# Performance work log

Hardware: AMD Instinct MI355X
Metric: run time of the kernel (lower is better)

Reference implementation:

```python
import jax, jax.numpy as jnp
import numpy as np

DEPTH = 6
H = 12
D = 768
FF = 4 * D
OUT_INDICES = (2, 5)
EPS = 1e-5


def layernorm(x, g, b):
    m = jnp.mean(x, axis=-1, keepdims=True)
    v = jnp.mean(jnp.square(x - m), axis=-1, keepdims=True)
    return (x - m) * jax.lax.rsqrt(v + EPS) * g + b


def setup_inputs() -> dict:
    key = jax.random.key(0)
    ks = jax.random.split(key, 8)
    B, N = 2, 1024
    s = 0.02
    inp = {
        "x": jax.random.normal(ks[0], (B, N, D), dtype=jnp.float32),
        "rel_bias": jax.random.normal(ks[1], (H, N, N), dtype=jnp.float32),
        "ln1_g": jnp.ones((DEPTH, D), jnp.float32),
        "ln1_b": jnp.zeros((DEPTH, D), jnp.float32),
        "qkv_w": jax.random.normal(ks[2], (DEPTH, D, 3 * D), dtype=jnp.float32) * s,
        "out_w": jax.random.normal(ks[3], (DEPTH, D, D), dtype=jnp.float32) * s,
        "out_b": jnp.zeros((DEPTH, D), jnp.float32),
        "ln2_g": jnp.ones((DEPTH, D), jnp.float32),
        "ln2_b": jnp.zeros((DEPTH, D), jnp.float32),
        "ff1_w": jax.random.normal(ks[4], (DEPTH, D, FF), dtype=jnp.float32) * s,
        "ff1_b": jnp.zeros((DEPTH, FF), jnp.float32),
        "ff2_w": jax.random.normal(ks[5], (DEPTH, FF, D), dtype=jnp.float32) * s,
        "ff2_b": jnp.zeros((DEPTH, D), jnp.float32),
        "lnf_g": jnp.ones((D,), jnp.float32),
        "lnf_b": jnp.zeros((D,), jnp.float32),
    }
    return inp


def reference(x, rel_bias, ln1_g, ln1_b, qkv_w, out_w, out_b, ln2_g, ln2_b,
              ff1_w, ff1_b, ff2_w, ff2_b, lnf_g, lnf_b):
    B, N, Dm = x.shape
    Dh = Dm // H
    scale = Dh ** -0.5
    kside = int(round(N ** 0.5))  # N is a perfect square (patch grid)
    feats = []
    for i in range(DEPTH):
        # --- attention block ---
        h = layernorm(x, ln1_g[i], ln1_b[i])
        qkv = h @ qkv_w[i]                                   # [B,N,3D]
        q, k, v = jnp.split(qkv, 3, axis=-1)
        q = q.reshape(B, N, H, Dh).transpose(0, 2, 1, 3)     # [B,H,N,Dh]
        k = k.reshape(B, N, H, Dh).transpose(0, 2, 1, 3)
        v = v.reshape(B, N, H, Dh).transpose(0, 2, 1, 3)
        scores = jnp.einsum('bhid,bhjd->bhij', q, k) * scale + rel_bias
        attn = jax.nn.softmax(scores, axis=-1)
        o = jnp.einsum('bhij,bhjd->bhid', attn, v)
        o = o.transpose(0, 2, 1, 3).reshape(B, N, Dm)
        x = x + (o @ out_w[i] + out_b[i])
        # --- FFN block ---
        h2 = layernorm(x, ln2_g[i], ln2_b[i])
        ff = jax.nn.gelu(h2 @ ff1_w[i] + ff1_b[i], approximate=False)
        x = x + (ff @ ff2_w[i] + ff2_b[i])
        if i in OUT_INDICES:
            feats.append(x.reshape(B, kside, kside, Dm).transpose(0, 3, 1, 2))
    xf = layernorm(x, lnf_g, lnf_b)
    return (xf, *feats)
```

## Files before the change

### kernel.cpp

```cpp
#include <hip/hip_runtime.h>
#include <hip/hip_bf16.h>

typedef unsigned short ushort_t;
typedef __attribute__((ext_vector_type(8))) __bf16 bf16x8;
typedef __attribute__((ext_vector_type(8))) unsigned short u16x8;
typedef __attribute__((ext_vector_type(4))) float f32x4;
typedef __attribute__((ext_vector_type(4))) unsigned int u32x4;

#define DEPTH 6
#define HEADS 12
#define DMODEL 768
#define FFDIM 3072
#define BATCH 2
#define SEQ 1024
#define ROWS (BATCH * SEQ)

static __device__ __forceinline__ ushort_t f2bf(float f) {
  unsigned u = __builtin_bit_cast(unsigned, f);
  u += 0x7fffu + ((u >> 16) & 1u);
  return (ushort_t)(u >> 16);
}
static __device__ __forceinline__ float bf2f(ushort_t v) {
  return __builtin_bit_cast(float, (unsigned)v << 16);
}

template <int MREP, int NREP, int EPI>
__global__ __launch_bounds__(256) void gemm_bt(
    const ushort_t* __restrict__ A, const ushort_t* __restrict__ Bt,
    int lda, int ldb, int K,
    void* __restrict__ out0, void* __restrict__ out1,
    const float* __restrict__ f0) {
  constexpr int BM = 32 * MREP;
  constexpr int BN = 32 * NREP;
  constexpr int CHA = BM / 32;
  constexpr int CHB = BN / 32;
  __shared__ ushort_t sA[2][BM * 64];
  __shared__ ushort_t sB[2][BN * 64];

  const int tid = threadIdx.x;
  const int lane = tid & 63;
  const int wid = tid >> 6;
  const int wm = wid >> 1, wn = wid & 1;

  int bx, by;
  {
    const int nb = gridDim.x * gridDim.y;
    const int bid = blockIdx.y * gridDim.x + blockIdx.x;
    const int q = nb >> 3;
    const int swz = (bid & 7) * q + (bid >> 3);
    bx = swz % gridDim.x;
    by = swz / gridDim.x;
  }

  const ushort_t* Ab = A + (long)bx * BM * lda;
  const ushort_t* Bb = Bt + (long)by * BN * ldb;

  const int srow = lane >> 3;
  const int scol = ((lane & 7) ^ srow) * 8;

  f32x4 acc[MREP][NREP];
#pragma unroll
  for (int m = 0; m < MREP; ++m)
#pragma unroll
    for (int n = 0; n < NREP; ++n) acc[m][n] = (f32x4){0.f, 0.f, 0.f, 0.f};

  const int fr = lane & 15;
  const int kq4 = lane >> 4;

  auto stage_tile = [&](int buf, int t) {
    const int k0 = t * 64;
#pragma unroll
    for (int j = 0; j < CHA; ++j) {
      const int c = wid * CHA + j;
      const ushort_t* src = Ab + (long)(c * 8 + srow) * lda + k0 + scol;
      __builtin_amdgcn_global_load_lds(
          (const __attribute__((address_space(1))) void*)src,
          (__attribute__((address_space(3))) void*)&sA[buf][c * 512], 16, 0, 0);
    }
#pragma unroll
    for (int j = 0; j < CHB; ++j) {
      const int c = wid * CHB + j;
      const ushort_t* src = Bb + (long)(c * 8 + srow) * ldb + k0 + scol;
      __builtin_amdgcn_global_load_lds(
          (const __attribute__((address_space(1))) void*)src,
          (__attribute__((address_space(3))) void*)&sB[buf][c * 512], 16, 0, 0);
    }
  };

  const int nt = K / 64;
  stage_tile(0, 0);
  for (int t = 0; t < nt; ++t) {
    const int cur = t & 1;
    asm volatile("s_waitcnt vmcnt(0)" ::: "memory");
    __builtin_amdgcn_s_barrier();
    if (t + 1 < nt) stage_tile(cur ^ 1, t + 1);
#pragma unroll
    for (int kk = 0; kk < 2; ++kk) {
      bf16x8 af[MREP], bfr[NREP];
#pragma unroll
      for (int m = 0; m < MREP; ++m) {
        const int row = wm * (MREP * 16) + m * 16 + fr;
        const int ch = (kk * 4 + kq4) ^ (row & 7);
        af[m] = *(const bf16x8*)&sA[cur][row * 64 + ch * 8];
      }
#pragma unroll
      for (int n = 0; n < NREP; ++n) {
        const int row = wn * (NREP * 16) + n * 16 + fr;
        const int ch = (kk * 4 + kq4) ^ (row & 7);
        bfr[n] = *(const bf16x8*)&sB[cur][row * 64 + ch * 8];
      }
#pragma unroll
      for (int m = 0; m < MREP; ++m)
#pragma unroll
        for (int n = 0; n < NREP; ++n)
          acc[m][n] = __builtin_amdgcn_mfma_f32_16x16x32_bf16(
              af[m], bfr[n], acc[m][n], 0, 0, 0);
    }
  }

  const long grow0 = (long)bx * BM + wm * (MREP * 16);
  const long gcol0 = (long)by * BN + wn * (NREP * 16);
  const int rr = (lane >> 4) * 4;
  const int cc = lane & 15;

#pragma unroll
  for (int m = 0; m < MREP; ++m) {
#pragma unroll
    for (int n = 0; n < NREP; ++n) {
#pragma unroll
      for (int r = 0; r < 4; ++r) {
        long row = grow0 + m * 16 + rr + r;
        long col = gcol0 + n * 16 + cc;
        float c = acc[m][n][r];
        if (EPI == 0) {
          ushort_t bv = f2bf(c);
          if (col < 1536) {
            ((ushort_t*)out0)[row * 2304 + col] = bv;
          } else {
            long h = (col - 1536) >> 6, d = (col - 1536) & 63;
            long b = row >> 10, i = row & 1023;
            ((ushort_t*)out1)[(((b * HEADS) + h) * 64 + d) * 1024 + i] = bv;
          }
        } else if (EPI == 3) {
          long idx = row * DMODEL + col;
          ((float*)out0)[idx] += c + f0[col];
        } else if (EPI == 4) {
          float t = c + f0[col];
          float g = 0.5f * t * (1.0f + erff(t * 0.70710678118f));
          ((ushort_t*)out0)[row * FFDIM + col] = f2bf(g);
        } else if (EPI == 5) {
          long idx = row * DMODEL + col;
          ((float*)out0)[idx] += c + f0[col];
        }
      }
    }
  }
}

__global__ __launch_bounds__(256) void pack_bias(const float* __restrict__ rel,
                                                 ushort_t* __restrict__ pb) {
  __shared__ ushort_t tile[1024];
  const int blk = blockIdx.x;
  const int t = blk & 15, qi = (blk >> 4) & 63, h = blk >> 10;
  const float* src = rel + ((size_t)h << 20) + (size_t)(qi * 16) * 1024 + t * 64;
  const int tid = threadIdx.x;
  const int kk = tid & 63;
#pragma unroll
  for (int it = 0; it < 4; ++it) {
    const int qr = (tid >> 6) * 4 + it;
    const float v = src[(size_t)qr * 1024 + kk];
    const int lane = (qr >> 2) * 16 + (kk & 15);
    const int idx = (kk >> 4) * 4 + (qr & 3);
    tile[lane * 16 + idx] = f2bf(v);
  }
  __syncthreads();
  ushort_t* dst = pb + (size_t)blk * 1024;
#pragma unroll
  for (int it = 0; it < 4; ++it) dst[it * 256 + tid] = tile[it * 256 + tid];
}

__global__ __launch_bounds__(128) void flash_attn(
    const ushort_t* __restrict__ qkv,
    const ushort_t* __restrict__ vt,
    const ushort_t* __restrict__ pbias,
    ushort_t* __restrict__ o) {
  __shared__ ushort_t sK[2][64 * 64];
  __shared__ ushort_t sV[2][64 * 64];
  __shared__ ushort_t sP[32 * 64];

  const int tid = threadIdx.x;
  const int lane = tid & 63;
  const int wid = tid >> 6;
  const int h = blockIdx.y, b = blockIdx.z;
  const int q0 = blockIdx.x * 32;
  const int qi = blockIdx.x * 2 + wid;

  const int fr = lane & 15;
  const int kq4 = lane >> 4;
  const int rr = kq4 * 4;
  const int cc = fr;

  const int srow = lane >> 3;
  const int scol = ((lane & 7) ^ srow) * 8;

  const ushort_t* qbase =
      qkv + (size_t)(b * 1024 + q0 + wid * 16 + fr) * 2304 + h * 64;
  bf16x8 qreg[2];
  qreg[0] = *(const bf16x8*)&qbase[kq4 * 8];
  qreg[1] = *(const bf16x8*)&qbase[32 + kq4 * 8];

  const ushort_t* Kbase = qkv + (size_t)(b * 1024) * 2304 + 768 + h * 64;
  const ushort_t* Vbase = vt + (size_t)((b * HEADS + h) * 64) * 1024;
  const ushort_t* pbb = pbias + (((size_t)h * 64 + qi) << 14) + lane * 16;

  f32x4 acc_o[4];
  float m_run[4], l_run[4];
#pragma unroll
  for (int n = 0; n < 4; ++n) acc_o[n] = (f32x4){0.f, 0.f, 0.f, 0.f};
#pragma unroll
  for (int r = 0; r < 4; ++r) { m_run[r] = -1e30f; l_run[r] = 0.f; }

  auto stage_kv = [&](int buf, int t) {
#pragma unroll
    for (int j = 0; j < 4; ++j) {
      const int c = wid * 4 + j;
      const ushort_t* src = Kbase + (size_t)(t * 64 + c * 8 + srow) * 2304 + scol;
      __builtin_amdgcn_global_load_lds(
          (const __attribute__((address_space(1))) void*)src,
          (__attribute__((address_space(3))) void*)&sK[buf][c * 512], 16, 0, 0);
    }
#pragma unroll
    for (int j = 0; j < 4; ++j) {
      const int c = wid * 4 + j;
      const ushort_t* src = Vbase + (size_t)(c * 8 + srow) * 1024 + t * 64 + scol;
      __builtin_amdgcn_global_load_lds(
          (const __attribute__((address_space(1))) void*)src,
          (__attribute__((address_space(3))) void*)&sV[buf][c * 512], 16, 0, 0);
    }
  };

  auto step = [&](int t, u16x8& bc0, u16x8& bc1, u16x8& bn0, u16x8& bn1) {
    const int cur = t & 1;
    asm volatile("s_waitcnt vmcnt(0)" ::: "memory");
    __builtin_amdgcn_s_barrier();
    if (t + 1 < 16) {
      stage_kv(cur ^ 1, t + 1);
      const ushort_t* pp = pbb + (size_t)(t + 1) * 1024;
      bn0 = *(const u16x8*)pp;
      bn1 = *(const u16x8*)(pp + 8);
    }

    f32x4 s[4];
#pragma unroll
    for (int n = 0; n < 4; ++n) s[n] = (f32x4){0.f, 0.f, 0.f, 0.f};
#pragma unroll
    for (int kk = 0; kk < 2; ++kk) {
#pragma unroll
      for (int n = 0; n < 4; ++n) {
        const int row = n * 16 + fr;
        const int ch = (kk * 4 + kq4) ^ (row & 7);
        bf16x8 kf = *(const bf16x8*)&sK[cur][row * 64 + ch * 8];
        s[n] =
            __builtin_amdgcn_mfma_f32_16x16x32_bf16(qreg[kk], kf, s[n], 0, 0, 0);
      }
    }

    float mr[4];
#pragma unroll
    for (int r = 0; r < 4; ++r) mr[r] = -1e30f;
#pragma unroll
    for (int n = 0; n < 4; ++n)
#pragma unroll
      for (int r = 0; r < 4; ++r) {
        const int idx = n * 4 + r;
        const float bv = bf2f(idx < 8 ? bc0[idx] : bc1[idx - 8]);
        float v = s[n][r] * 0.125f + bv;
        s[n][r] = v;
        mr[r] = fmaxf(mr[r], v);
      }
#pragma unroll
    for (int o_ = 1; o_ < 16; o_ <<= 1)
#pragma unroll
      for (int r = 0; r < 4; ++r) mr[r] = fmaxf(mr[r], __shfl_xor(mr[r], o_));

    float escale[4], psum[4];
#pragma unroll
    for (int r = 0; r < 4; ++r) {
      float mn = fmaxf(m_run[r], mr[r]);
      escale[r] = __expf(m_run[r] - mn);
      m_run[r] = mn;
      psum[r] = 0.f;
    }
#pragma unroll
    for (int n = 0; n < 4; ++n)
#pragma unroll
      for (int r = 0; r < 4; ++r) {
        float p = __expf(s[n][r] - m_run[r]);
        psum[r] += p;
        const int prow = wid * 16 + rr + r;
        const int pcol = n * 16 + cc;
        sP[prow * 64 + (((pcol >> 3) ^ (prow & 7)) << 3) + (pcol & 7)] = f2bf(p);
      }
#pragma unroll
    for (int o_ = 1; o_ < 16; o_ <<= 1)
#pragma unroll
      for (int r = 0; r < 4; ++r) psum[r] += __shfl_xor(psum[r], o_);
#pragma unroll
    for (int r = 0; r < 4; ++r) l_run[r] = l_run[r] * escale[r] + psum[r];

    asm volatile("s_waitcnt lgkmcnt(0)" ::: "memory");
    __builtin_amdgcn_s_barrier();

#pragma unroll
    for (int n = 0; n < 4; ++n)
#pragma unroll
      for (int r = 0; r < 4; ++r) acc_o[n][r] *= escale[r];
#pragma unroll
    for (int kk = 0; kk < 2; ++kk) {
      const int prow = wid * 16 + fr;
      const int pch = (kk * 4 + kq4) ^ (prow & 7);
      bf16x8 pf = *(const bf16x8*)&sP[prow * 64 + pch * 8];
#pragma unroll
      for (int n = 0; n < 4; ++n) {
        const int vrow = n * 16 + fr;
        const int vch = (kk * 4 + kq4) ^ (vrow & 7);
        bf16x8 vf = *(const bf16x8*)&sV[cur][vrow * 64 + vch * 8];
        acc_o[n] =
            __builtin_amdgcn_mfma_f32_16x16x32_bf16(pf, vf, acc_o[n], 0, 0, 0);
      }
    }
  };

  u16x8 bA0, bA1, bB0, bB1;
  bA0 = *(const u16x8*)pbb;
  bA1 = *(const u16x8*)(pbb + 8);
  stage_kv(0, 0);
  for (int tt = 0; tt < 16; tt += 2) {
    step(tt, bA0, bA1, bB0, bB1);
    step(tt + 1, bB0, bB1, bA0, bA1);
  }

  ushort_t* ob = o + (size_t)(b * 1024 + q0 + wid * 16) * 768 + h * 64;
#pragma unroll
  for (int r = 0; r < 4; ++r) {
    const float rinv = 1.f / l_run[r];
#pragma unroll
    for (int n = 0; n < 4; ++n)
      ob[(size_t)(rr + r) * 768 + n * 16 + cc] = f2bf(acc_o[n][r] * rinv);
  }
}

__global__ __launch_bounds__(256) void transpose_cast(
    const float* __restrict__ in, ushort_t* __restrict__ out, int R, int C) {
  __shared__ float t[32][33];
  const float* ip = in + (long)blockIdx.z * R * C;
  ushort_t* op = out + (long)blockIdx.z * R * C;
  int c0 = blockIdx.x * 32, r0 = blockIdx.y * 32;
  int tx = threadIdx.x;
  for (int i = threadIdx.y; i < 32; i += 8)
    t[i][tx] = ip[(long)(r0 + i) * C + c0 + tx];
  __syncthreads();
  for (int i = threadIdx.y; i < 32; i += 8)
    op[(long)(c0 + i) * R + r0 + tx] = f2bf(t[tx][i]);
}

__global__ __launch_bounds__(256) void ln_kernel(
    const float* __restrict__ x, const float* __restrict__ g,
    const float* __restrict__ b, void* __restrict__ out, int out_f32) {
  int row = blockIdx.x;
  int tid = threadIdx.x;
  int lane = tid & 63, wid = tid >> 6;
  const float* xr = x + (long)row * DMODEL;
  float v0 = xr[tid], v1 = xr[tid + 256], v2 = xr[tid + 512];
  float s = v0 + v1 + v2;
  __shared__ float red[8];
  for (int o = 32; o; o >>= 1) s += __shfl_xor(s, o);
  if (!lane) red[wid] = s;
  __syncthreads();
  float mean = (red[0] + red[1] + red[2] + red[3]) * (1.f / 768.f);
  float d0 = v0 - mean, d1 = v1 - mean, d2 = v2 - mean;
  float q = d0 * d0 + d1 * d1 + d2 * d2;
  for (int o = 32; o; o >>= 1) q += __shfl_xor(q, o);
  if (!lane) red[4 + wid] = q;
  __syncthreads();
  float var = (red[4] + red[5] + red[6] + red[7]) * (1.f / 768.f);
  float rs = rsqrtf(var + 1e-5f);
  float y0 = d0 * rs * g[tid] + b[tid];
  float y1 = d1 * rs * g[tid + 256] + b[tid + 256];
  float y2 = d2 * rs * g[tid + 512] + b[tid + 512];
  if (out_f32) {
    float* o_ = (float*)out + (long)row * DMODEL;
    o_[tid] = y0; o_[tid + 256] = y1; o_[tid + 512] = y2;
  } else {
    ushort_t* o_ = (ushort_t*)out + (long)row * DMODEL;
    o_[tid] = f2bf(y0); o_[tid + 256] = f2bf(y1); o_[tid + 512] = f2bf(y2);
  }
}

__global__ __launch_bounds__(256) void feat_kernel(const float* __restrict__ x,
                                                   float* __restrict__ out) {
  __shared__ float t[32][33];
  const float* xp = x + (long)blockIdx.z * SEQ * DMODEL;
  float* op = out + (long)blockIdx.z * DMODEL * SEQ;
  int n0 = blockIdx.x * 32, c0 = blockIdx.y * 32;
  int tx = threadIdx.x;
  for (int i = threadIdx.y; i < 32; i += 8)
    t[i][tx] = xp[(long)(n0 + i) * DMODEL + c0 + tx];
  __syncthreads();
  for (int i = threadIdx.y; i < 32; i += 8)
    op[(long)(c0 + i) * SEQ + n0 + tx] = t[tx][i];
}

extern "C" void kernel_launch(void* const* d_in, const int* in_sizes, int n_in,
                              void* d_out, int out_size, void* d_ws,
                              size_t ws_size, hipStream_t stream) {
  const float* x_in   = (const float*)d_in[0];
  const float* rel    = (const float*)d_in[1];
  const float* ln1_g  = (const float*)d_in[2];
  const float* ln1_b  = (const float*)d_in[3];
  const float* qkv_w  = (const float*)d_in[4];
  const float* out_w  = (const float*)d_in[5];
  const float* out_b  = (const float*)d_in[6];
  const float* ln2_g  = (const float*)d_in[7];
  const float* ln2_b  = (const float*)d_in[8];
  const float* ff1_w  = (const float*)d_in[9];
  const float* ff1_b  = (const float*)d_in[10];
  const float* ff2_w  = (const float*)d_in[11];
  const float* ff2_b  = (const float*)d_in[12];
  const float* lnf_g  = (const float*)d_in[13];
  const float* lnf_b  = (const float*)d_in[14];
  float* out = (float*)d_out;

  char* w = (char*)d_ws;
  ushort_t* wq_t = (ushort_t*)w; w += (size_t)DEPTH * 2304 * 768 * 2;
  ushort_t* wo_t = (ushort_t*)w; w += (size_t)DEPTH * 768 * 768 * 2;
  ushort_t* wf1_t = (ushort_t*)w; w += (size_t)DEPTH * 3072 * 768 * 2;
  ushort_t* wf2_t = (ushort_t*)w; w += (size_t)DEPTH * 768 * 3072 * 2;
  float* xb = (float*)w; w += (size_t)ROWS * DMODEL * 4;
  ushort_t* hb = (ushort_t*)w; w += (size_t)ROWS * DMODEL * 2;
  ushort_t* qkvb = (ushort_t*)w; w += (size_t)ROWS * 2304 * 2;
  ushort_t* vt = (ushort_t*)w; w += (size_t)BATCH * HEADS * 64 * 1024 * 2;
  ushort_t* ob = (ushort_t*)w; w += (size_t)ROWS * DMODEL * 2;
  ushort_t* ffb = (ushort_t*)w; w += (size_t)ROWS * FFDIM * 2;
  ushort_t* pbias = (ushort_t*)w; w += (size_t)HEADS * 1024 * 1024 * 2;

  dim3 tb(32, 8);
  transpose_cast<<<dim3(2304 / 32, 768 / 32, DEPTH), tb, 0, stream>>>(
      qkv_w, wq_t, 768, 2304);
  transpose_cast<<<dim3(768 / 32, 768 / 32, DEPTH), tb, 0, stream>>>(
      out_w, wo_t, 768, 768);
  transpose_cast<<<dim3(3072 / 32, 768 / 32, DEPTH), tb, 0, stream>>>(
      ff1_w, wf1_t, 768, 3072);
  transpose_cast<<<dim3(768 / 32, 3072 / 32, DEPTH), tb, 0, stream>>>(
      ff2_w, wf2_t, 3072, 768);
  pack_bias<<<HEADS * 64 * 16, 256, 0, stream>>>(rel, pbias);

  hipMemcpyAsync(xb, x_in, (size_t)ROWS * DMODEL * 4, hipMemcpyDeviceToDevice,
                 stream);

  for (int i = 0; i < DEPTH; ++i) {
    ln_kernel<<<ROWS, 256, 0, stream>>>(xb, ln1_g + i * 768, ln1_b + i * 768,
                                        hb, 0);
    gemm_bt<1, 2, 0><<<dim3(64, 36), 256, 0, stream>>>(
        hb, wq_t + (size_t)i * 2304 * 768, 768, 768, 768, qkvb, vt, nullptr);
    flash_attn<<<dim3(32, HEADS, BATCH), 128, 0, stream>>>(qkvb, vt, pbias, ob);
    gemm_bt<1, 2, 3><<<dim3(64, 12), 256, 0, stream>>>(
        ob, wo_t + (size_t)i * 768 * 768, 768, 768, 768, xb, nullptr,
        out_b + i * 768);
    ln_kernel<<<ROWS, 256, 0, stream>>>(xb, ln2_g + i * 768, ln2_b + i * 768,
                                        hb, 0);
    gemm_bt<1, 2, 4><<<dim3(64, 48), 256, 0, stream>>>(
        hb, wf1_t + (size_t)i * 3072 * 768, 768, 768, 768, ffb, nullptr,
        ff1_b + i * 3072);
    gemm_bt<1, 2, 5><<<dim3(64, 12), 256, 0, stream>>>(
        ffb, wf2_t + (size_t)i * 768 * 3072, 3072, 3072, 3072, xb, nullptr,
        ff2_b + i * 768);
    if (i == 2)
      feat_kernel<<<dim3(32, 24, 2), tb, 0, stream>>>(xb, out + 1572864);
    if (i == 5)
      feat_kernel<<<dim3(32, 24, 2), tb, 0, stream>>>(xb, out + 2 * 1572864);
  }
  ln_kernel<<<ROWS, 256, 0, stream>>>(xb, lnf_g, lnf_b, out, 1);
}
```

Before: 930.7 us.

## Fuse layernorm into GEMM A-staging using residual-epilogue row statistics

The residual-add GEMM epilogues now accumulate per-row sum and sum-of-squares into a stats buffer with shuffles and atomics. The QKV and FF1 GEMMs normalize fp32 activations on the fly while staging the A tile into LDS, which removes the two standalone layernorm kernels per layer and the bf16 intermediate buffer. Those two GEMMs also move to a 64-row tile. The trade-offs are register-path A loads in place of direct global-to-LDS loads, redundant normalization of A across column blocks, and a one-pass variance (E[x²]−mean²) that is less numerically stable.

```diff
diff --git a/kernel.cpp b/kernel.cpp
--- a/kernel.cpp
+++ b/kernel.cpp
@@ -24,12 +24,14 @@
   return __builtin_bit_cast(float, (unsigned)v << 16);
 }
 
-template <int MREP, int NREP, int EPI>
+template <int MREP, int NREP, int EPI, int LNA>
 __global__ __launch_bounds__(256) void gemm_bt(
-    const ushort_t* __restrict__ A, const ushort_t* __restrict__ Bt,
+    const void* __restrict__ Ap, const ushort_t* __restrict__ Bt,
     int lda, int ldb, int K,
     void* __restrict__ out0, void* __restrict__ out1,
-    const float* __restrict__ f0) {
+    const float* __restrict__ f0,
+    const float* __restrict__ st_in, const float* __restrict__ lng,
+    const float* __restrict__ lnb, float* __restrict__ st_out) {
   constexpr int BM = 32 * MREP;
   constexpr int BN = 32 * NREP;
   constexpr int CHA = BM / 32;
@@ -52,7 +54,12 @@
     by = swz / gridDim.x;
   }
 
-  const ushort_t* Ab = A + (long)bx * BM * lda;
+  const ushort_t* Ab = nullptr;
+  const float* Af = nullptr;
+  if constexpr (LNA)
+    Af = (const float*)Ap + (long)bx * BM * lda;
+  else
+    Ab = (const ushort_t*)Ap + (long)bx * BM * lda;
   const ushort_t* Bb = Bt + (long)by * BN * ldb;
 
   const int srow = lane >> 3;
@@ -72,10 +79,34 @@
 #pragma unroll
     for (int j = 0; j < CHA; ++j) {
       const int c = wid * CHA + j;
-      const ushort_t* src = Ab + (long)(c * 8 + srow) * lda + k0 + scol;
-      __builtin_amdgcn_global_load_lds(
-          (const __attribute__((address_space(1))) void*)src,
-          (__attribute__((address_space(3))) void*)&sA[buf][c * 512], 16, 0, 0);
+      if constexpr (LNA) {
+        const int row = c * 8 + srow;
+        const float* xr = Af + (long)row * lda + k0 + scol;
+        f32x4 xa = *(const f32x4*)xr;
+        f32x4 xc = *(const f32x4*)(xr + 4);
+        f32x4 g0 = *(const f32x4*)&lng[k0 + scol];
+        f32x4 g1 = *(const f32x4*)&lng[k0 + scol + 4];
+        f32x4 b0 = *(const f32x4*)&lnb[k0 + scol];
+        f32x4 b1 = *(const f32x4*)&lnb[k0 + scol + 4];
+        const float* st = st_in + (size_t)(bx * BM + row) * 2;
+        float mean = st[0] * (1.f / 768.f);
+        float var = st[1] * (1.f / 768.f) - mean * mean;
+        float rstd = rsqrtf(var + 1e-5f);
+        u16x8 pk;
+#pragma unroll
+        for (int jj = 0; jj < 4; ++jj)
+          pk[jj] = f2bf((xa[jj] - mean) * rstd * g0[jj] + b0[jj]);
+#pragma unroll
+        for (int jj = 0; jj < 4; ++jj)
+          pk[4 + jj] = f2bf((xc[jj] - mean) * rstd * g1[jj] + b1[jj]);
+        *(u16x8*)&sA[buf][c * 512 + lane * 8] = pk;
+      } else {
+        const ushort_t* src = Ab + (long)(c * 8 + srow) * lda + k0 + scol;
+        __builtin_amdgcn_global_load_lds(
+            (const __attribute__((address_space(1))) void*)src,
+            (__attribute__((address_space(3))) void*)&sA[buf][c * 512], 16, 0,
+            0);
+      }
     }
 #pragma unroll
     for (int j = 0; j < CHB; ++j) {
@@ -91,7 +122,10 @@
   stage_tile(0, 0);
   for (int t = 0; t < nt; ++t) {
     const int cur = t & 1;
-    asm volatile("s_waitcnt vmcnt(0)" ::: "memory");
+    if constexpr (LNA)
+      asm volatile("s_waitcnt vmcnt(0) lgkmcnt(0)" ::: "memory");
+    else
+      asm volatile("s_waitcnt vmcnt(0)" ::: "memory");
     __builtin_amdgcn_s_barrier();
     if (t + 1 < nt) stage_tile(cur ^ 1, t + 1);
 #pragma unroll
@@ -122,6 +156,8 @@
   const long gcol0 = (long)by * BN + wn * (NREP * 16);
   const int rr = (lane >> 4) * 4;
   const int cc = lane & 15;
+
+  float rs[4] = {0.f, 0.f, 0.f, 0.f}, rq[4] = {0.f, 0.f, 0.f, 0.f};
 
 #pragma unroll
   for (int m = 0; m < MREP; ++m) {
@@ -141,19 +177,61 @@
             long b = row >> 10, i = row & 1023;
             ((ushort_t*)out1)[(((b * HEADS) + h) * 64 + d) * 1024 + i] = bv;
           }
-        } else if (EPI == 3) {
+        } else if (EPI == 3 || EPI == 5) {
           long idx = row * DMODEL + col;
-          ((float*)out0)[idx] += c + f0[col];
+          float nv = ((float*)out0)[idx] + c + f0[col];
+          ((float*)out0)[idx] = nv;
+          rs[r] += nv;
+          rq[r] += nv * nv;
         } else if (EPI == 4) {
           float t = c + f0[col];
           float g = 0.5f * t * (1.0f + erff(t * 0.70710678118f));
           ((ushort_t*)out0)[row * FFDIM + col] = f2bf(g);
-        } else if (EPI == 5) {
-          long idx = row * DMODEL + col;
-          ((float*)out0)[idx] += c + f0[col];
         }
       }
     }
+  }
+
+  if constexpr (EPI == 3 || EPI == 5) {
+#pragma unroll
+    for (int r = 0; r < 4; ++r) {
+      float s = rs[r], q = rq[r];
+#pragma unroll
+      for (int mask = 1; mask < 16; mask <<= 1) {
+        s += __shfl_xor(s, mask);
+        q += __shfl_xor(q, mask);
+      }
+      if (cc == 0) {
+        long row = grow0 + rr + r;
+        atomicAdd(&st_out[row * 2], s);
+        atomicAdd(&st_out[row * 2 + 1], q);
+      }
+    }
+  }
+}
+
+__global__ __launch_bounds__(64) void ln_stats(const float* __restrict__ x,
+                                               float* __restrict__ st) {
+  const size_t row = blockIdx.x;
+  const int t = threadIdx.x;
+  const float* xr = x + row * DMODEL;
+  float s = 0.f, q = 0.f;
+#pragma unroll
+  for (int i = 0; i < 3; ++i) {
+    f32x4 v = *(const f32x4*)&xr[t * 4 + i * 256];
+#pragma unroll
+    for (int j = 0; j < 4; ++j) {
+      s += v[j];
+      q += v[j] * v[j];
+    }
+  }
+  for (int mask = 1; mask < 64; mask <<= 1) {
+    s += __shfl_xor(s, mask);
+    q += __shfl_xor(q, mask);
+  }
+  if (t == 0) {
+    st[row * 2] = s;
+    st[row * 2 + 1] = q;
   }
 }
 
@@ -437,12 +515,12 @@
   ushort_t* wf1_t = (ushort_t*)w; w += (size_t)DEPTH * 3072 * 768 * 2;
   ushort_t* wf2_t = (ushort_t*)w; w += (size_t)DEPTH * 768 * 3072 * 2;
   float* xb = (float*)w; w += (size_t)ROWS * DMODEL * 4;
-  ushort_t* hb = (ushort_t*)w; w += (size_t)ROWS * DMODEL * 2;
   ushort_t* qkvb = (ushort_t*)w; w += (size_t)ROWS * 2304 * 2;
   ushort_t* vt = (ushort_t*)w; w += (size_t)BATCH * HEADS * 64 * 1024 * 2;
   ushort_t* ob = (ushort_t*)w; w += (size_t)ROWS * DMODEL * 2;
   ushort_t* ffb = (ushort_t*)w; w += (size_t)ROWS * FFDIM * 2;
   ushort_t* pbias = (ushort_t*)w; w += (size_t)HEADS * 1024 * 1024 * 2;
+  float* stats = (float*)w; w += (size_t)(2 * DEPTH + 1) * ROWS * 2 * 4;
 
   dim3 tb(32, 8);
   transpose_cast<<<dim3(2304 / 32, 768 / 32, DEPTH), tb, 0, stream>>>(
@@ -455,26 +533,28 @@
       ff2_w, wf2_t, 3072, 768);
   pack_bias<<<HEADS * 64 * 16, 256, 0, stream>>>(rel, pbias);
 
+  hipMemsetAsync(stats, 0, (size_t)(2 * DEPTH + 1) * ROWS * 2 * 4, stream);
   hipMemcpyAsync(xb, x_in, (size_t)ROWS * DMODEL * 4, hipMemcpyDeviceToDevice,
                  stream);
+  ln_stats<<<ROWS, 64, 0, stream>>>(xb, stats);
 
   for (int i = 0; i < DEPTH; ++i) {
-    ln_kernel<<<ROWS, 256, 0, stream>>>(xb, ln1_g + i * 768, ln1_b + i * 768,
-                                        hb, 0);
-    gemm_bt<1, 2, 0><<<dim3(64, 36), 256, 0, stream>>>(
-        hb, wq_t + (size_t)i * 2304 * 768, 768, 768, 768, qkvb, vt, nullptr);
+    float* st_ln1 = stats + (size_t)(2 * i) * ROWS * 2;
+    float* st_ln2 = stats + (size_t)(2 * i + 1) * ROWS * 2;
+    float* st_nx1 = stats + (size_t)(2 * i + 2) * ROWS * 2;
+    gemm_bt<2, 2, 0, 1><<<dim3(32, 36), 256, 0, stream>>>(
+        xb, wq_t + (size_t)i * 2304 * 768, 768, 768, 768, qkvb, vt, nullptr,
+        st_ln1, ln1_g + i * 768, ln1_b + i * 768, nullptr);
     flash_attn<<<dim3(32, HEADS, BATCH), 128, 0, stream>>>(qkvb, vt, pbias, ob);
-    gemm_bt<1, 2, 3><<<dim3(64, 12), 256, 0, stream>>>(
+    gemm_bt<1, 2, 3, 0><<<dim3(64, 12), 256, 0, stream>>>(
         ob, wo_t + (size_t)i * 768 * 768, 768, 768, 768, xb, nullptr,
-        out_b + i * 768);
-    ln_kernel<<<ROWS, 256, 0, stream>>>(xb, ln2_g + i * 768, ln2_b + i * 768,
-                                        hb, 0);
-    gemm_bt<1, 2, 4><<<dim3(64, 48), 256, 0, stream>>>(
-        hb, wf1_t + (size_t)i * 3072 * 768, 768, 768, 768, ffb, nullptr,
-        ff1_b + i * 3072);
-    gemm_bt<1, 2, 5><<<dim3(64, 12), 256, 0, stream>>>(
+        out_b + i * 768, nullptr, nullptr, nullptr, st_ln2);
+    gemm_bt<2, 2, 4, 1><<<dim3(32, 48), 256, 0, stream>>>(
+        xb, wf1_t + (size_t)i * 3072 * 768, 768, 768, 768, ffb, nullptr,
+        ff1_b + i * 3072, st_ln2, ln2_g + i * 768, ln2_b + i * 768, nullptr);
+    gemm_bt<1, 2, 5, 0><<<dim3(64, 12), 256, 0, stream>>>(
         ffb, wf2_t + (size_t)i * 768 * 3072, 3072, 3072, 3072, xb, nullptr,
-        ff2_b + i * 768);
+        ff2_b + i * 768, nullptr, nullptr, nullptr, st_nx1);
     if (i == 2)
       feat_kernel<<<dim3(32, 24, 2), tb, 0, stream>>>(xb, out + 1572864);
     if (i == 5)
```

Result: slower. 1.115 ms (+19.8%).
